# Kernel optimization log

Hardware: AMD Instinct MI355X
Metric: run time of the kernel (lower is better)

Reference implementation:

```python
import jax, jax.numpy as jnp
import numpy as np


def setup_inputs() -> dict:
    key = jax.random.key(0)
    ks = jax.random.split(key, 13)
    HID = 256
    N = 2 * HID                      # hidden_dim * 2
    B_DOC, S, T_K = 32, 40, 64      # docs, sentences/doc, max words/sentence
    B_SENT = B_DOC * S               # total sentences = sum(sent_lens)
    MAX_DOC_LEN = S * T_K
    f = jnp.float32
    sc = jnp.float32(0.05)
    sent_lens = jnp.full((B_DOC,), S, dtype=jnp.int32)
    inp = {
        "s_t_hat": jax.random.normal(ks[0], (B_DOC, N), f),
        "encoder_outputs": jax.random.normal(ks[1], (B_SENT, T_K, N), f),
        "encoder_feature": jax.random.normal(ks[2], (B_SENT * T_K, N), f) * jnp.float32(0.5),
        "seq_lens2": jax.random.randint(ks[3], (B_SENT,), T_K // 2, T_K + 1, dtype=jnp.int32),
        "sent_s_t_hat": jax.random.normal(ks[4], (B_DOC, N), f),
        "sent_enc_outputs": jax.random.normal(ks[5], (B_DOC, S, N), f),
        "sent_enc_feature": jax.random.normal(ks[6], (B_DOC * S, N), f) * jnp.float32(0.5),
        "sent_enc_padding_mask": (jnp.arange(S)[None, :] < sent_lens[:, None]).astype(f),
        "sent_lens": sent_lens,
        "max_doc_len": MAX_DOC_LEN,
        "coverage": jnp.zeros((B_SENT, T_K), f),
        "Wd": jax.random.normal(ks[7], (N, N), f) * sc,
        "bd": jax.random.normal(ks[8], (N,), f) * sc,
        "v_w": jax.random.normal(ks[9], (N,), f) * sc,
        "Wsd": jax.random.normal(ks[10], (N, N), f) * sc,
        "bsd": jax.random.normal(ks[11], (N,), f) * sc,
        "sv_w": jax.random.normal(ks[12], (N,), f) * sc,
    }
    return inp


def _excl_cumsum(x):
    return jnp.cumsum(x) - x


def reference(s_t_hat, encoder_outputs, encoder_feature, seq_lens2, sent_s_t_hat,
              sent_enc_outputs, sent_enc_feature, sent_enc_padding_mask, sent_lens,
              max_doc_len, coverage, Wd, bd, v_w, Wsd, bsd, sv_w):
    B_SENT, T_K, N = encoder_outputs.shape
    B_DOC, S, _ = sent_enc_outputs.shape
    dtype = encoder_outputs.dtype

    # sentence s -> owning doc (replaces first Python loop: broadcast dec_fea per doc)
    doc_ids = jnp.repeat(jnp.arange(B_DOC), sent_lens, total_repeat_length=B_SENT)

    # ---- word-level additive attention over each sentence ----
    dec_fea = s_t_hat @ Wd + bd                              # [B_DOC, N]
    att = jnp.tanh(encoder_feature.reshape(B_SENT, T_K, N) + dec_fea[doc_ids][:, None, :])
    scores = att @ v_w                                        # [B_SENT, T_K]
    w_mask = (jnp.arange(T_K)[None, :] < seq_lens2[:, None]).astype(dtype)
    w_attn_ = jax.nn.softmax(scores, axis=1) * w_mask
    w_attn = w_attn_ / w_attn_.sum(1, keepdims=True)          # [B_SENT, T_K]

    # ---- sentence-level additive attention over each doc ----
    sent_dec_fea = sent_s_t_hat @ Wsd + bsd                   # [B_DOC, N]
    sent_att = jnp.tanh(sent_enc_feature.reshape(B_DOC, S, N) + sent_dec_fea[:, None, :])
    sent_scores = sent_att @ sv_w                             # [B_DOC, S]
    sent_attn_ = jax.nn.softmax(sent_scores, axis=1) * sent_enc_padding_mask
    sent_attn_dist = sent_attn_ / sent_attn_.sum(1, keepdims=True)

    # ---- ragged flatten: scatter valid words of each sentence into its doc stream ----
    sent_start = _excl_cumsum(sent_lens)                      # first sentence idx per doc
    sent_local = jnp.arange(B_SENT) - sent_start[doc_ids]     # sentence pos within doc
    mult_attn = sent_attn_dist[doc_ids, sent_local][:, None] * w_attn  # [B_SENT, T_K]

    word_cum = _excl_cumsum(seq_lens2)                        # global word offsets
    doc_word_off = word_cum - word_cum[sent_start[doc_ids]]   # offset within doc
    pos = doc_word_off[:, None] + jnp.arange(T_K)[None, :]    # [B_SENT, T_K]
    valid = jnp.arange(T_K)[None, :] < seq_lens2[:, None]
    flat = jnp.where(valid, doc_ids[:, None] * max_doc_len + pos, B_DOC * max_doc_len)
    flat = flat.reshape(-1)

    enc_output2 = (jnp.zeros((B_DOC * max_doc_len, N), dtype)
                   .at[flat].set(encoder_outputs.reshape(-1, N), mode="drop")
                   .reshape(B_DOC, max_doc_len, N))
    attn_dist_sw = (jnp.zeros((B_DOC * max_doc_len,), dtype)
                    .at[flat].set(mult_attn.reshape(-1), mode="drop")
                    .reshape(B_DOC, max_doc_len))

    c_t = jnp.einsum("bl,bln->bn", attn_dist_sw, enc_output2)  # [B_DOC, N]
    return (c_t, attn_dist_sw, coverage, sent_attn_dist)
```

## Files before the change

kernel.cpp:

```cpp
#include <hip/hip_runtime.h>
#include <hip/hip_bf16.h>
#include <math.h>

#define B_DOC 32
#define S_MAX 40
#define T_K 64
#define N_DIM 512
#define B_SENT (B_DOC * S_MAX)
#define MAXDOC (S_MAX * T_K)
#define KCHUNK 4

__device__ __forceinline__ float fast_tanh(float x) {
    float e = __expf(2.0f * x);
    return 1.0f - 2.0f * __builtin_amdgcn_rcpf(e + 1.0f);
}

__global__ __launch_bounds__(256) void prep_fea_kernel(
        const int* __restrict__ seq_lens2, const int* __restrict__ sent_lens,
        const float* __restrict__ s_t_hat, const float* __restrict__ sent_s_t_hat,
        const float* __restrict__ Wd, const float* __restrict__ bd,
        const float* __restrict__ Wsd, const float* __restrict__ bsd,
        float* __restrict__ fea_part,
        int* __restrict__ doc_ids, int* __restrict__ sent_local,
        int* __restrict__ doc_word_off, int* __restrict__ sent_start_g,
        int* __restrict__ doc_words_total) {
    int tid = threadIdx.x;
    if (blockIdx.x == 256) {
        __shared__ int ss[B_DOC + 1];
        __shared__ int wc[B_SENT + 1];
        __shared__ int wsum[4];
        int lane = tid & 63, w = tid >> 6;

        int ls[5];
        #pragma unroll
        for (int k = 0; k < 5; ++k) ls[k] = seq_lens2[tid * 5 + k];
        int sum = ls[0] + ls[1] + ls[2] + ls[3] + ls[4];

        int scan = sum;
        #pragma unroll
        for (int off = 1; off < 64; off <<= 1) {
            int v = __shfl_up(scan, off, 64);
            if (lane >= off) scan += v;
        }
        if (lane == 63) wsum[w] = scan;

        if (w == 0) {
            int sl = (lane < B_DOC) ? sent_lens[lane] : 0;
            int sc2 = sl;
            #pragma unroll
            for (int off = 1; off < 64; off <<= 1) {
                int v = __shfl_up(sc2, off, 64);
                if (lane >= off) sc2 += v;
            }
            if (lane < B_DOC) ss[lane + 1] = sc2;
            if (lane == 0) ss[0] = 0;
        }
        __syncthreads();

        int wbase = 0;
        for (int i = 0; i < w; ++i) wbase += wsum[i];
        int excl = wbase + scan - sum;
        #pragma unroll
        for (int k = 0; k < 5; ++k) { wc[tid * 5 + k] = excl; excl += ls[k]; }
        if (tid == 255) wc[B_SENT] = excl;
        __syncthreads();

        if (tid <= B_DOC) sent_start_g[tid] = ss[tid];
        if (tid < B_DOC) doc_words_total[tid] = wc[ss[tid + 1]] - wc[ss[tid]];

        for (int i = tid; i < B_SENT; i += 256) {
            int lo = 0, hi = B_DOC - 1;
            while (lo < hi) { int mid = (lo + hi + 1) >> 1; if (ss[mid] <= i) lo = mid; else hi = mid - 1; }
            doc_ids[i] = lo;
            sent_local[i] = i - ss[lo];
            doc_word_off[i] = wc[i] - wc[ss[lo]];
        }
    } else {
        int blk = blockIdx.x;
        int c = blk & (KCHUNK - 1);
        int b = (blk >> 2) & 31;
        int m = blk >> 7;
        const int KC = N_DIM / KCHUNK;
        const float* x = (m ? sent_s_t_hat : s_t_hat) + b * N_DIM + c * KC;
        const float* W = (m ? Wsd : Wd) + (size_t)c * KC * N_DIM;
        const float* bias = (m ? bsd : bd);
        float* out = fea_part + ((size_t)(m * 32 + b) * KCHUNK + c) * N_DIM;
        __shared__ float xs[128];
        if (tid < KC) xs[tid] = x[tid];
        __syncthreads();
        float a0 = 0.f, a1 = 0.f;
        if (c == 0) { a0 = bias[tid]; a1 = bias[tid + 256]; }
        #pragma unroll 8
        for (int k = 0; k < KC; ++k) {
            float xv = xs[k];
            a0 = fmaf(xv, W[k * N_DIM + tid], a0);
            a1 = fmaf(xv, W[k * N_DIM + tid + 256], a1);
        }
        out[tid] = a0;
        out[tid + 256] = a1;
    }
}

__global__ __launch_bounds__(256) void sent_attn_kernel(
        const float* __restrict__ sef, const float* __restrict__ fea_part,
        const float* __restrict__ sv_w, const float* __restrict__ mask,
        float* __restrict__ out_sent) {
    int b = blockIdx.x;
    __shared__ float df[N_DIM];
    __shared__ float vw[N_DIM];
    __shared__ float sc[S_MAX];
    int tid = threadIdx.x;
    const float* fp = fea_part + (size_t)(32 + b) * KCHUNK * N_DIM;
    for (int i = tid; i < N_DIM; i += 256) {
        df[i] = fp[i] + fp[N_DIM + i] + fp[2 * N_DIM + i] + fp[3 * N_DIM + i];
        vw[i] = sv_w[i];
    }
    __syncthreads();
    int w = tid >> 6, lane = tid & 63;
    const float4* sef4 = (const float4*)(sef + (size_t)b * S_MAX * N_DIM);
    const float4* df4 = (const float4*)df;
    const float4* vw4 = (const float4*)vw;
    for (int t = w; t < S_MAX; t += 4) {
        float acc = 0.0f;
        #pragma unroll
        for (int j = 0; j < 2; ++j) {
            int n4 = lane + 64 * j;
            float4 e = sef4[t * 128 + n4];
            float4 d = df4[n4];
            float4 v = vw4[n4];
            acc = fmaf(v.x, fast_tanh(e.x + d.x), acc);
            acc = fmaf(v.y, fast_tanh(e.y + d.y), acc);
            acc = fmaf(v.z, fast_tanh(e.z + d.z), acc);
            acc = fmaf(v.w, fast_tanh(e.w + d.w), acc);
        }
        #pragma unroll
        for (int off = 32; off >= 1; off >>= 1) acc += __shfl_xor(acc, off, 64);
        if (lane == 0) sc[t] = acc;
    }
    __syncthreads();
    if (tid < 64) {
        bool valid = tid < S_MAX;
        float x = valid ? sc[tid] : -INFINITY;
        float m = x;
        #pragma unroll
        for (int off = 32; off >= 1; off >>= 1) m = fmaxf(m, __shfl_xor(m, off, 64));
        float mk = valid ? mask[b * S_MAX + tid] : 0.0f;
        float e = valid ? __expf(x - m) * mk : 0.0f;
        float ssum = e;
        #pragma unroll
        for (int off = 32; off >= 1; off >>= 1) ssum += __shfl_xor(ssum, off, 64);
        if (valid) out_sent[b * S_MAX + tid] = e / ssum;
    }
}

__global__ __launch_bounds__(256, 4) void fused_kernel(
        const float* __restrict__ ef, const float* __restrict__ eo,
        const float* __restrict__ fea_part, const float* __restrict__ v_w,
        const float* __restrict__ sent_attn, const int* __restrict__ seq_lens2,
        const int* __restrict__ doc_ids, const int* __restrict__ sent_local,
        const int* __restrict__ doc_word_off, const int* __restrict__ sent_start,
        const int* __restrict__ doc_words_total, const int* __restrict__ mdl,
        const float* __restrict__ cov_in,
        float* __restrict__ part, float* __restrict__ out_attn,
        float* __restrict__ out_cov) {
    int s = blockIdx.x;
    int tid = threadIdx.x;
    int w = tid >> 6, lane = tid & 63;
    __shared__ float sc[T_K];
    __shared__ float wm[4], wl[4];
    __shared__ float4 red[4][128];

    int doc = doc_ids[s];
    int len = seq_lens2[s];
    int maxdoc = mdl[0];

    const float4* fp4 = (const float4*)(fea_part + (size_t)doc * KCHUNK * N_DIM);
    float4 d0 = fp4[lane], d1 = fp4[64 + lane];
    #pragma unroll
    for (int c = 1; c < KCHUNK; ++c) {
        float4 a = fp4[c * 128 + lane], b = fp4[c * 128 + 64 + lane];
        d0.x += a.x; d0.y += a.y; d0.z += a.z; d0.w += a.w;
        d1.x += b.x; d1.y += b.y; d1.z += b.z; d1.w += b.w;
    }
    const float4* vw4 = (const float4*)v_w;
    float4 v0 = vw4[lane], v1 = vw4[64 + lane];

    if (tid < T_K) out_cov[s * T_K + tid] = cov_in[s * T_K + tid];

    const float4* ef4 = (const float4*)(ef + (size_t)s * T_K * N_DIM);
    const float4* eo4 = (const float4*)(eo + (size_t)s * T_K * N_DIM);

    float m_w = -INFINITY, l_w = 0.0f;
    float4 O0 = {0.f, 0.f, 0.f, 0.f}, O1 = {0.f, 0.f, 0.f, 0.f};

    float4 ea0, ea1;
    if (w < len) { ea0 = ef4[w * 128 + lane]; ea1 = ef4[w * 128 + 64 + lane]; }
    for (int t = w; t < len; t += 4) {
        float4 p0 = eo4[t * 128 + lane];
        float4 p1 = eo4[t * 128 + 64 + lane];
        float4 eb0, eb1;
        int tn = t + 4;
        if (tn < len) { eb0 = ef4[tn * 128 + lane]; eb1 = ef4[tn * 128 + 64 + lane]; }
        float acc;
        acc  = v0.x * fast_tanh(ea0.x + d0.x);
        acc = fmaf(v0.y, fast_tanh(ea0.y + d0.y), acc);
        acc = fmaf(v0.z, fast_tanh(ea0.z + d0.z), acc);
        acc = fmaf(v0.w, fast_tanh(ea0.w + d0.w), acc);
        acc = fmaf(v1.x, fast_tanh(ea1.x + d1.x), acc);
        acc = fmaf(v1.y, fast_tanh(ea1.y + d1.y), acc);
        acc = fmaf(v1.z, fast_tanh(ea1.z + d1.z), acc);
        acc = fmaf(v1.w, fast_tanh(ea1.w + d1.w), acc);
        #pragma unroll
        for (int off = 32; off >= 1; off >>= 1) acc += __shfl_xor(acc, off, 64);
        if (lane == 0) sc[t] = acc;
        if (acc > m_w) {
            float r = __expf(m_w - acc);
            l_w *= r;
            O0.x *= r; O0.y *= r; O0.z *= r; O0.w *= r;
            O1.x *= r; O1.y *= r; O1.z *= r; O1.w *= r;
            m_w = acc;
        }
        float p = __expf(acc - m_w);
        l_w += p;
        O0.x = fmaf(p, p0.x, O0.x); O0.y = fmaf(p, p0.y, O0.y);
        O0.z = fmaf(p, p0.z, O0.z); O0.w = fmaf(p, p0.w, O0.w);
        O1.x = fmaf(p, p1.x, O1.x); O1.y = fmaf(p, p1.y, O1.y);
        O1.z = fmaf(p, p1.z, O1.z); O1.w = fmaf(p, p1.w, O1.w);
        ea0 = eb0; ea1 = eb1;
    }

    if (lane == 0) { wm[w] = m_w; wl[w] = l_w; }
    __syncthreads();
    float m = fmaxf(fmaxf(wm[0], wm[1]), fmaxf(wm[2], wm[3]));
    float l = __expf(wm[0] - m) * wl[0] + __expf(wm[1] - m) * wl[1]
            + __expf(wm[2] - m) * wl[2] + __expf(wm[3] - m) * wl[3];
    float fw = __expf(m_w - m);
    red[w][lane].x = O0.x * fw; red[w][lane].y = O0.y * fw;
    red[w][lane].z = O0.z * fw; red[w][lane].w = O0.w * fw;
    red[w][64 + lane].x = O1.x * fw; red[w][64 + lane].y = O1.y * fw;
    red[w][64 + lane].z = O1.z * fw; red[w][64 + lane].w = O1.w * fw;
    float sa = sent_attn[doc * S_MAX + sent_local[s]];
    float inv = sa / l;
    __syncthreads();
    if (tid < 128) {
        float4 a = red[0][tid], b = red[1][tid], c = red[2][tid], d = red[3][tid];
        float4 r = {(a.x + b.x + c.x + d.x) * inv, (a.y + b.y + c.y + d.y) * inv,
                    (a.z + b.z + c.z + d.z) * inv, (a.w + b.w + c.w + d.w) * inv};
        ((float4*)(part + (size_t)s * N_DIM))[tid] = r;
    }
    if (tid < T_K && tid < len) {
        float mu = sa * __expf(sc[tid] - m) / l;
        out_attn[(size_t)doc * maxdoc + doc_word_off[s] + tid] = mu;
    }
    if (s + 1 == sent_start[doc + 1]) {
        int dwt = doc_words_total[doc];
        for (int i = dwt + tid; i < maxdoc; i += 256)
            out_attn[(size_t)doc * maxdoc + i] = 0.0f;
    }
}

__global__ __launch_bounds__(128) void reduce_kernel(
        const float* __restrict__ part, const int* __restrict__ sent_start,
        float* __restrict__ c_t) {
    int b = blockIdx.x;
    int nq = threadIdx.x;
    int st = sent_start[b], en = sent_start[b + 1];
    float4 acc = {0.f, 0.f, 0.f, 0.f};
    for (int s = st; s < en; ++s) {
        float4 p = ((const float4*)(part + (size_t)s * N_DIM))[nq];
        acc.x += p.x; acc.y += p.y; acc.z += p.z; acc.w += p.w;
    }
    ((float4*)(c_t + (size_t)b * N_DIM))[nq] = acc;
}

extern "C" void kernel_launch(void* const* d_in, const int* in_sizes, int n_in,
                              void* d_out, int out_size, void* d_ws, size_t ws_size,
                              hipStream_t stream) {
    const float* s_t_hat        = (const float*)d_in[0];
    const float* encoder_out    = (const float*)d_in[1];
    const float* encoder_feat   = (const float*)d_in[2];
    const int*   seq_lens2      = (const int*)d_in[3];
    const float* sent_s_t_hat   = (const float*)d_in[4];
    const float* sent_enc_feat  = (const float*)d_in[6];
    const float* sent_pad_mask  = (const float*)d_in[7];
    const int*   sent_lens      = (const int*)d_in[8];
    const int*   max_doc_len    = (const int*)d_in[9];
    const float* coverage       = (const float*)d_in[10];
    const float* Wd             = (const float*)d_in[11];
    const float* bd             = (const float*)d_in[12];
    const float* v_w            = (const float*)d_in[13];
    const float* Wsd            = (const float*)d_in[14];
    const float* bsd            = (const float*)d_in[15];
    const float* sv_w           = (const float*)d_in[16];

    float* out      = (float*)d_out;
    float* o_ct     = out;
    float* o_attn   = out + B_DOC * N_DIM;
    float* o_cov    = o_attn + B_DOC * MAXDOC;
    float* o_sent   = o_cov + B_SENT * T_K;

    float* ws          = (float*)d_ws;
    float* fea_part    = ws;
    float* part        = ws + 131072;
    int*   ints        = (int*)(ws + 131072 + 655360);
    int*   doc_ids     = ints;
    int*   sent_local  = ints + B_SENT;
    int*   doc_w_off   = ints + 2 * B_SENT;
    int*   sent_start  = ints + 3 * B_SENT;
    int*   doc_wtot    = ints + 3 * B_SENT + 33;

    prep_fea_kernel<<<257, 256, 0, stream>>>(seq_lens2, sent_lens, s_t_hat,
                                             sent_s_t_hat, Wd, bd, Wsd, bsd,
                                             fea_part, doc_ids, sent_local,
                                             doc_w_off, sent_start, doc_wtot);
    sent_attn_kernel<<<B_DOC, 256, 0, stream>>>(sent_enc_feat, fea_part, sv_w,
                                                sent_pad_mask, o_sent);
    fused_kernel<<<B_SENT, 256, 0, stream>>>(encoder_feat, encoder_out, fea_part,
                                             v_w, o_sent, seq_lens2, doc_ids,
                                             sent_local, doc_w_off, sent_start,
                                             doc_wtot, max_doc_len, coverage,
                                             part, o_attn, o_cov);
    reduce_kernel<<<B_DOC, 128, 0, stream>>>(part, sent_start, o_ct);
}
```

Before: 77.47 us.

## Split each wave into half-wave row pairs and drop online softmax max tracking

Each 64-lane wave now handles two timesteps at once, one per 32-lane half, so each lane holds four float4 slices. That shortens the shuffle reduction to five steps and halves the loop trip count. The running max and rescaling are removed, and raw exp(score) is used on the assumption that scores are bounded by the sum of |v_w|, which also removes a __syncthreads. The risk is overflow if the scores grow large, plus higher register pressure from four float4 accumulators and prefetch buffers.

```diff
diff --git a/kernel.cpp b/kernel.cpp
--- a/kernel.cpp
+++ b/kernel.cpp
@@ -166,90 +166,119 @@
     int s = blockIdx.x;
     int tid = threadIdx.x;
     int w = tid >> 6, lane = tid & 63;
+    int h = lane >> 5, sub = lane & 31;
     __shared__ float sc[T_K];
-    __shared__ float wm[4], wl[4];
-    __shared__ float4 red[4][128];
+    __shared__ float wl[4];
+    __shared__ __align__(16) float4 red[4][128];
 
     int doc = doc_ids[s];
     int len = seq_lens2[s];
     int maxdoc = mdl[0];
 
     const float4* fp4 = (const float4*)(fea_part + (size_t)doc * KCHUNK * N_DIM);
-    float4 d0 = fp4[lane], d1 = fp4[64 + lane];
+    const float4* vw4 = (const float4*)v_w;
+    float4 d[4], v[4];
     #pragma unroll
-    for (int c = 1; c < KCHUNK; ++c) {
-        float4 a = fp4[c * 128 + lane], b = fp4[c * 128 + 64 + lane];
-        d0.x += a.x; d0.y += a.y; d0.z += a.z; d0.w += a.w;
-        d1.x += b.x; d1.y += b.y; d1.z += b.z; d1.w += b.w;
-    }
-    const float4* vw4 = (const float4*)v_w;
-    float4 v0 = vw4[lane], v1 = vw4[64 + lane];
+    for (int k = 0; k < 4; ++k) {
+        int j = sub + 32 * k;
+        float4 a = fp4[j], b = fp4[128 + j], c = fp4[256 + j], e = fp4[384 + j];
+        d[k].x = a.x + b.x + c.x + e.x;
+        d[k].y = a.y + b.y + c.y + e.y;
+        d[k].z = a.z + b.z + c.z + e.z;
+        d[k].w = a.w + b.w + c.w + e.w;
+        v[k] = vw4[j];
+    }
 
     if (tid < T_K) out_cov[s * T_K + tid] = cov_in[s * T_K + tid];
 
-    const float4* ef4 = (const float4*)(ef + (size_t)s * T_K * N_DIM);
-    const float4* eo4 = (const float4*)(eo + (size_t)s * T_K * N_DIM);
-
-    float m_w = -INFINITY, l_w = 0.0f;
-    float4 O0 = {0.f, 0.f, 0.f, 0.f}, O1 = {0.f, 0.f, 0.f, 0.f};
-
-    float4 ea0, ea1;
-    if (w < len) { ea0 = ef4[w * 128 + lane]; ea1 = ef4[w * 128 + 64 + lane]; }
-    for (int t = w; t < len; t += 4) {
-        float4 p0 = eo4[t * 128 + lane];
-        float4 p1 = eo4[t * 128 + 64 + lane];
-        float4 eb0, eb1;
-        int tn = t + 4;
-        if (tn < len) { eb0 = ef4[tn * 128 + lane]; eb1 = ef4[tn * 128 + 64 + lane]; }
-        float acc;
-        acc  = v0.x * fast_tanh(ea0.x + d0.x);
-        acc = fmaf(v0.y, fast_tanh(ea0.y + d0.y), acc);
-        acc = fmaf(v0.z, fast_tanh(ea0.z + d0.z), acc);
-        acc = fmaf(v0.w, fast_tanh(ea0.w + d0.w), acc);
-        acc = fmaf(v1.x, fast_tanh(ea1.x + d1.x), acc);
-        acc = fmaf(v1.y, fast_tanh(ea1.y + d1.y), acc);
-        acc = fmaf(v1.z, fast_tanh(ea1.z + d1.z), acc);
-        acc = fmaf(v1.w, fast_tanh(ea1.w + d1.w), acc);
-        #pragma unroll
-        for (int off = 32; off >= 1; off >>= 1) acc += __shfl_xor(acc, off, 64);
-        if (lane == 0) sc[t] = acc;
-        if (acc > m_w) {
-            float r = __expf(m_w - acc);
-            l_w *= r;
-            O0.x *= r; O0.y *= r; O0.z *= r; O0.w *= r;
-            O1.x *= r; O1.y *= r; O1.z *= r; O1.w *= r;
-            m_w = acc;
-        }
-        float p = __expf(acc - m_w);
+    const float4* ef4 = (const float4*)ef + (size_t)s * T_K * 128;
+    const float4* eo4 = (const float4*)eo + (size_t)s * T_K * 128;
+
+    float l_w = 0.0f;
+    float4 O[4];
+    #pragma unroll
+    for (int k = 0; k < 4; ++k) O[k] = (float4){0.f, 0.f, 0.f, 0.f};
+
+    int t = 2 * w;
+    float4 ea[4];
+    {
+        int row = t + h;
+        #pragma unroll
+        for (int k = 0; k < 4; ++k) ea[k] = ef4[row * 128 + sub + 32 * k];
+    }
+    for (; t < len; t += 8) {
+        int row = t + h;
+        float4 p4[4];
+        #pragma unroll
+        for (int k = 0; k < 4; ++k) p4[k] = eo4[row * 128 + sub + 32 * k];
+        float4 eb[4];
+        int tn = t + 8;
+        if (tn < len) {
+            int rown = tn + h;
+            #pragma unroll
+            for (int k = 0; k < 4; ++k) eb[k] = ef4[rown * 128 + sub + 32 * k];
+        }
+        float a0, a1, a2, a3;
+        a0  = v[0].x * fast_tanh(ea[0].x + d[0].x);
+        a1  = v[1].x * fast_tanh(ea[1].x + d[1].x);
+        a2  = v[2].x * fast_tanh(ea[2].x + d[2].x);
+        a3  = v[3].x * fast_tanh(ea[3].x + d[3].x);
+        a0 = fmaf(v[0].y, fast_tanh(ea[0].y + d[0].y), a0);
+        a1 = fmaf(v[1].y, fast_tanh(ea[1].y + d[1].y), a1);
+        a2 = fmaf(v[2].y, fast_tanh(ea[2].y + d[2].y), a2);
+        a3 = fmaf(v[3].y, fast_tanh(ea[3].y + d[3].y), a3);
+        a0 = fmaf(v[0].z, fast_tanh(ea[0].z + d[0].z), a0);
+        a1 = fmaf(v[1].z, fast_tanh(ea[1].z + d[1].z), a1);
+        a2 = fmaf(v[2].z, fast_tanh(ea[2].z + d[2].z), a2);
+        a3 = fmaf(v[3].z, fast_tanh(ea[3].z + d[3].z), a3);
+        a0 = fmaf(v[0].w, fast_tanh(ea[0].w + d[0].w), a0);
+        a1 = fmaf(v[1].w, fast_tanh(ea[1].w + d[1].w), a1);
+        a2 = fmaf(v[2].w, fast_tanh(ea[2].w + d[2].w), a2);
+        a3 = fmaf(v[3].w, fast_tanh(ea[3].w + d[3].w), a3);
+        float acc = (a0 + a1) + (a2 + a3);
+        #pragma unroll
+        for (int off = 16; off >= 1; off >>= 1) acc += __shfl_xor(acc, off, 64);
+        bool valid = (t + h) < len;
+        if (sub == 0 && valid) sc[t + h] = acc;
+        float p = valid ? __expf(acc) : 0.0f;
         l_w += p;
-        O0.x = fmaf(p, p0.x, O0.x); O0.y = fmaf(p, p0.y, O0.y);
-        O0.z = fmaf(p, p0.z, O0.z); O0.w = fmaf(p, p0.w, O0.w);
-        O1.x = fmaf(p, p1.x, O1.x); O1.y = fmaf(p, p1.y, O1.y);
-        O1.z = fmaf(p, p1.z, O1.z); O1.w = fmaf(p, p1.w, O1.w);
-        ea0 = eb0; ea1 = eb1;
-    }
-
-    if (lane == 0) { wm[w] = m_w; wl[w] = l_w; }
+        #pragma unroll
+        for (int k = 0; k < 4; ++k) {
+            O[k].x = fmaf(p, p4[k].x, O[k].x);
+            O[k].y = fmaf(p, p4[k].y, O[k].y);
+            O[k].z = fmaf(p, p4[k].z, O[k].z);
+            O[k].w = fmaf(p, p4[k].w, O[k].w);
+        }
+        #pragma unroll
+        for (int k = 0; k < 4; ++k) ea[k] = eb[k];
+    }
+
+    l_w += __shfl_xor(l_w, 32, 64);
+    #pragma unroll
+    for (int k = 0; k < 4; ++k) {
+        O[k].x += __shfl_xor(O[k].x, 32, 64);
+        O[k].y += __shfl_xor(O[k].y, 32, 64);
+        O[k].z += __shfl_xor(O[k].z, 32, 64);
+        O[k].w += __shfl_xor(O[k].w, 32, 64);
+    }
+    if (lane == 0) wl[w] = l_w;
+    if (h == 0) {
+        #pragma unroll
+        for (int k = 0; k < 4; ++k) red[w][sub + 32 * k] = O[k];
+    }
     __syncthreads();
-    float m = fmaxf(fmaxf(wm[0], wm[1]), fmaxf(wm[2], wm[3]));
-    float l = __expf(wm[0] - m) * wl[0] + __expf(wm[1] - m) * wl[1]
-            + __expf(wm[2] - m) * wl[2] + __expf(wm[3] - m) * wl[3];
-    float fw = __expf(m_w - m);
-    red[w][lane].x = O0.x * fw; red[w][lane].y = O0.y * fw;
-    red[w][lane].z = O0.z * fw; red[w][lane].w = O0.w * fw;
-    red[w][64 + lane].x = O1.x * fw; red[w][64 + lane].y = O1.y * fw;
-    red[w][64 + lane].z = O1.z * fw; red[w][64 + lane].w = O1.w * fw;
+
+    float l = (wl[0] + wl[1]) + (wl[2] + wl[3]);
     float sa = sent_attn[doc * S_MAX + sent_local[s]];
     float inv = sa / l;
-    __syncthreads();
     if (tid < 128) {
-        float4 a = red[0][tid], b = red[1][tid], c = red[2][tid], d = red[3][tid];
-        float4 r = {(a.x + b.x + c.x + d.x) * inv, (a.y + b.y + c.y + d.y) * inv,
-                    (a.z + b.z + c.z + d.z) * inv, (a.w + b.w + c.w + d.w) * inv};
+        float4 a = red[0][tid], b = red[1][tid], c = red[2][tid], e = red[3][tid];
+        float4 r = {(a.x + b.x + c.x + e.x) * inv, (a.y + b.y + c.y + e.y) * inv,
+                    (a.z + b.z + c.z + e.z) * inv, (a.w + b.w + c.w + e.w) * inv};
         ((float4*)(part + (size_t)s * N_DIM))[tid] = r;
     }
     if (tid < T_K && tid < len) {
-        float mu = sa * __expf(sc[tid] - m) / l;
+        float mu = sa * __expf(sc[tid]) / l;
         out_attn[(size_t)doc * maxdoc + doc_word_off[s] + tid] = mu;
     }
     if (s + 1 == sent_start[doc + 1]) {
```

After: 78.04 us. No clear change (+0.7%).
